# Performance work log

Measured on AMD Instinct MI355X. Metric: run time of the kernel, lower is better.

Reference implementation:

```python
import jax, jax.numpy as jnp
import numpy as np

jax.config.update("jax_enable_x64", True)

B, N, M_EQ, D_INEQ = 64, 128, 32, 64
RHO = 1.0
THRES = 1e-5
MAX_ITERS = 5000  # safety cap (original loops until relative objective change <= 1e-5)


def setup_inputs() -> dict:
    key = jax.random.key(0)
    kL, kq, kG, kA, kx0, ks = jax.random.split(key, 6)
    L = jax.random.normal(kL, (B, N, N))
    Q = jnp.einsum('bij,bkj->bik', L, L) / N + jnp.eye(N)  # SPD, well-conditioned
    q = jax.random.normal(kq, (B, N))
    G = jax.random.normal(kG, (B, D_INEQ, N))
    A = jax.random.normal(kA, (B, M_EQ, N))
    x0 = jax.random.normal(kx0, (B, N))
    slack = jax.random.uniform(ks, (B, D_INEQ)) + 0.1
    h = jnp.einsum('bdn,bn->bd', G, x0) + slack  # strictly feasible ineq
    b = jnp.einsum('bmn,bn->bm', A, x0)          # feasible eq
    f32 = jnp.float32
    return {"Q": Q.astype(f32), "q": q.astype(f32), "G": G.astype(f32),
            "h": h.astype(f32), "A": A.astype(f32), "b": b.astype(f32)}


def _alt_diff_batch(Q, q, G, h, A, b):
    """Batched Alt-Diff ADMM QP solve; returns (x [B,n], dx/dq [B,n,n])."""
    Bb, n = q.shape
    d = h.shape[1]
    m = b.shape[1]
    dt = Q.dtype
    AtA = jnp.einsum('bmi,bmj->bij', A, A)
    GtG = jnp.einsum('bdi,bdj->bij', G, G)
    R = -jnp.linalg.inv(Q + RHO * AtA + RHO * GtG)
    ATb = RHO * jnp.einsum('bmn,bm->bn', A, b)
    GTh = RHO * jnp.einsum('bdn,bd->bn', G, h)
    eye = jnp.eye(n, dtype=dt)

    def obj(x):
        return 0.5 * jnp.einsum('bi,bij,bj->b', x, Q, x) + jnp.einsum('bi,bi->b', q, x)

    init = dict(
        xk=jnp.zeros((Bb, n), dt), sk=jnp.zeros((Bb, d), dt),
        lamb=jnp.zeros((Bb, m), dt), nu=jnp.zeros((Bb, d), dt),
        dxk=jnp.zeros((Bb, n, n), dt), dsk=jnp.zeros((Bb, d, n), dt),
        dlamb=jnp.zeros((Bb, m, n), dt), dnu=jnp.zeros((Bb, d, n), dt),
        res_prev=jnp.full((Bb,), 1000.0, dt),   # res = [1000, -100] init
        res_cur=jnp.full((Bb,), -100.0, dt),
        done=jnp.zeros((Bb,), bool),
        it=jnp.zeros((), jnp.int32),
    )

    def cond(s):
        return jnp.logical_and(jnp.any(~s["done"]), s["it"] < MAX_ITERS)

    def body(s):
        xk = jnp.einsum('bij,bj->bi', R,
                        q + jnp.einsum('bmn,bm->bn', A, s["lamb"])
                          + jnp.einsum('bdn,bd->bn', G, s["nu"]) - ATb
                          + RHO * jnp.einsum('bdn,bd->bn', G, s["sk"]) - GTh)
        dxk = jnp.einsum('bij,bjk->bik', R,
                         eye + jnp.einsum('bmn,bmk->bnk', A, s["dlamb"])
                             + jnp.einsum('bdn,bdk->bnk', G, s["dnu"])
                             + RHO * jnp.einsum('bdn,bdk->bnk', G, s["dsk"]))
        Gx = jnp.einsum('bdn,bn->bd', G, xk)
        sk = jax.nn.relu(-(1.0 / RHO) * s["nu"] - (Gx - h))
        sgn = (sk > 0).astype(dt)  # sgn applied to already-relu'd sk, as in source
        dsk = (-1.0 / RHO) * sgn[:, :, None] * (s["dnu"] + RHO * jnp.einsum('bdn,bnk->bdk', G, dxk))
        lamb = s["lamb"] + RHO * (jnp.einsum('bmn,bn->bm', A, xk) - b)
        dlamb = s["dlamb"] + RHO * jnp.einsum('bmn,bnk->bmk', A, dxk)
        nu = s["nu"] + RHO * (Gx + sk - h)
        dnu = s["dnu"] + RHO * (jnp.einsum('bdn,bnk->bdk', G, dxk) + dsk)
        res_new = obj(xk)

        keep = s["done"]

        def sel(old, new):
            mask = keep.reshape((-1,) + (1,) * (new.ndim - 1))
            return jnp.where(mask, old, new)

        res_prev = jnp.where(keep, s["res_prev"], s["res_cur"])
        res_cur = jnp.where(keep, s["res_cur"], res_new)
        done = keep | (jnp.abs((res_cur - res_prev) / res_prev) <= THRES)
        return dict(
            xk=sel(s["xk"], xk), sk=sel(s["sk"], sk),
            lamb=sel(s["lamb"], lamb), nu=sel(s["nu"], nu),
            dxk=sel(s["dxk"], dxk), dsk=sel(s["dsk"], dsk),
            dlamb=sel(s["dlamb"], dlamb), dnu=sel(s["dnu"], dnu),
            res_prev=res_prev, res_cur=res_cur, done=done, it=s["it"] + 1,
        )

    final = jax.lax.while_loop(cond, body, init)
    return final["xk"], final["dxk"]


def reference(Q, q, G, h, A, b):
    out_dtype = q.dtype
    f64 = jnp.float64
    x, _dx = _alt_diff_batch(Q.astype(f64), q.astype(f64), G.astype(f64),
                             h.astype(f64), A.astype(f64), b.astype(f64))
    return x.astype(out_dtype)
```

## Files before the change

### kernel.cpp

```cpp
#include <hip/hip_runtime.h>

#define NN 128
#define ME 32
#define DI 64
#define NZ 96
#define ROWD 130
#define MAXIT 5000

#define OFF_UN 16640
#define ROWB  (OFF_UN)
#define COLB  (OFF_UN + 256)
#define PPK   (OFF_UN)
#define ZEXL  (OFF_UN + 512)
#define ZEXH  (OFF_UN + 640)
#define TVX   (OFF_UN + 704)
#define TV16  (OFF_UN + 832)
#define FLG   (OFF_UN + 864)
#define YBUF  (OFF_UN)
#define KBUF  (OFF_UN + 1536)
#define CPART (OFF_UN + 1024)
#define VP    (OFF_UN + 1280)
#define BASEV (OFF_UN + 1792)
#define QBV   (OFF_UN + 1888)
#define FPART (OFF_UN + 1024)
#define RHSV  (OFF_UN + 1280)
#define XPART (OFF_UN + 1408)
#define CB    (OFF_UN + 2688)
#define QBUF  (OFF_UN + 2816)
#define V1    (OFF_UN + 2944)
#define V2    (OFF_UN + 3072)
#define HB    (OFF_UN + 3200)
#define BB    (OFF_UN + 3264)
#define CST   (OFF_UN + 3296)
#define ZBF   (OFF_UN + 3304)
#define LDS_DBL (OFF_UN + 3400)

typedef __attribute__((ext_vector_type(2))) float f32x2;

__device__ __forceinline__ float rlf(float v, int lane) {
  return __uint_as_float((unsigned)__builtin_amdgcn_readlane((int)__float_as_uint(v), lane));
}
__device__ __forceinline__ f32x2 fma2(f32x2 a, f32x2 b, f32x2 c) {
  return __builtin_elementwise_fma(a, b, c);
}

#define MV2(PA, ZS, L0) {                                                  \
    f32x2 z0 = { rlf(ZS, L0), rlf(ZS, (L0)+1) };                           \
    A0 = fma2(Kp[PA], z0, A0); B0 = fma2(Kp2[PA], z0, B0);                 \
    f32x2 z1 = { rlf(ZS, (L0)+2), rlf(ZS, (L0)+3) };                       \
    A1 = fma2(Kp[(PA)+1], z1, A1); B1 = fma2(Kp2[(PA)+1], z1, B1); }

__global__ __launch_bounds__(320, 1) void altdiff_kernel(
    const float* __restrict__ Qg, const float* __restrict__ qg,
    const float* __restrict__ Gg, const float* __restrict__ hg,
    const float* __restrict__ Ag, const float* __restrict__ bg,
    float* __restrict__ out)
{
  extern __shared__ double ldsd[];

  const int bidx = blockIdx.x;
  const int tid  = threadIdx.x;
  const int w    = tid >> 6;
  const int l    = tid & 63;
  const int lm   = l & 31;
  const int ia   = tid & 127;
  const int hh   = tid >> 7;

  const float* Qb = Qg + (size_t)bidx * NN * NN;
  const float* Ab = Ag + (size_t)bidx * ME * NN;
  const float* Gb = Gg + (size_t)bidx * DI * NN;
  const float* qb = qg + (size_t)bidx * NN;
  const float* hb = hg + (size_t)bidx * DI;
  const float* bv = bg + (size_t)bidx * ME;

  if (tid < DI) ldsd[HB + tid] = (double)hb[tid];
  else if (tid < DI + ME) ldsd[BB + tid - DI] = (double)bv[tid - DI];
  if (tid >= 128 && tid < 256) ldsd[QBUF + tid - 128] = (double)qb[tid - 128];

  const int r = tid >> 4, c = tid & 15;
  double acc[8][8];

  if (tid < 256) {
    const float4* Q4 = (const float4*)Qb;
#pragma unroll
    for (int rr = 0; rr < 8; ++rr) {
      float4 q0 = Q4[((8*r+rr) << 5) + 2*c];
      float4 q1 = Q4[((8*r+rr) << 5) + 2*c + 1];
      acc[rr][0]=(double)q0.x; acc[rr][1]=(double)q0.y; acc[rr][2]=(double)q0.z; acc[rr][3]=(double)q0.w;
      acc[rr][4]=(double)q1.x; acc[rr][5]=(double)q1.y; acc[rr][6]=(double)q1.z; acc[rr][7]=(double)q1.w;
    }
    const float4* A4 = (const float4*)Ab;
    for (int m = 0; m < ME; ++m) {
      float4 u0 = A4[(m << 5) + 2*r], u1 = A4[(m << 5) + 2*r + 1];
      float4 v0 = A4[(m << 5) + 2*c], v1 = A4[(m << 5) + 2*c + 1];
      double uu[8] = {(double)u0.x,(double)u0.y,(double)u0.z,(double)u0.w,
                      (double)u1.x,(double)u1.y,(double)u1.z,(double)u1.w};
      double vv[8] = {(double)v0.x,(double)v0.y,(double)v0.z,(double)v0.w,
                      (double)v1.x,(double)v1.y,(double)v1.z,(double)v1.w};
#pragma unroll
      for (int rr = 0; rr < 8; ++rr)
#pragma unroll
        for (int cc = 0; cc < 8; ++cc)
          acc[rr][cc] = fma(uu[rr], vv[cc], acc[rr][cc]);
    }
    const float4* G4 = (const float4*)Gb;
    for (int d = 0; d < DI; ++d) {
      float4 u0 = G4[(d << 5) + 2*r], u1 = G4[(d << 5) + 2*r + 1];
      float4 v0 = G4[(d << 5) + 2*c], v1 = G4[(d << 5) + 2*c + 1];
      double uu[8] = {(double)u0.x,(double)u0.y,(double)u0.z,(double)u0.w,
                      (double)u1.x,(double)u1.y,(double)u1.z,(double)u1.w};
      double vv[8] = {(double)v0.x,(double)v0.y,(double)v0.z,(double)v0.w,
                      (double)v1.x,(double)v1.y,(double)v1.z,(double)v1.w};
#pragma unroll
      for (int rr = 0; rr < 8; ++rr)
#pragma unroll
        for (int cc = 0; cc < 8; ++cc)
          acc[rr][cc] = fma(uu[rr], vv[cc], acc[rr][cc]);
    }
  }

  if (tid < 256) {
    if (r == 0) {
#pragma unroll
      for (int cc = 0; cc < 8; ++cc) ldsd[ROWB + 8*c + cc] = acc[0][cc];
    }
    if (c == 0) {
#pragma unroll
      for (int rr = 0; rr < 8; ++rr) ldsd[COLB + 8*r + rr] = acc[rr][0];
    }
  }
  __syncthreads();
  for (int k = 0; k < NN; ++k) {
    if (tid < 256) {
      const int pb = (k & 1) << 7;
      const int krt = k >> 3, kcl = k & 7;
      double rowk[8], colv[8];
#pragma unroll
      for (int cc = 0; cc < 8; ++cc) rowk[cc] = ldsd[ROWB + pb + 8*c + cc];
#pragma unroll
      for (int rr = 0; rr < 8; ++rr) colv[rr] = ldsd[COLB + pb + 8*r + rr];
      const double dkk  = ldsd[ROWB + pb + k];
      const double rcpd = 1.0 / dkk;
      double rdv[8];
#pragma unroll
      for (int cc = 0; cc < 8; ++cc) rdv[cc] = rowk[cc] * rcpd;
      const bool pivR = (r == krt), pivC = (c == krt);
#pragma unroll
      for (int rr = 0; rr < 8; ++rr) {
        const double cv = colv[rr] * rcpd;
        const bool pr = pivR && (rr == kcl);
#pragma unroll
        for (int cc = 0; cc < 8; ++cc) {
          double gen = fma(-cv, rowk[cc], acc[rr][cc]);
          acc[rr][cc] = pr ? rdv[cc] : gen;
        }
      }
      if (pivC) {
#pragma unroll
        for (int cc = 0; cc < 8; ++cc) if (cc == kcl) {
#pragma unroll
          for (int rr = 0; rr < 8; ++rr) {
            const bool pr2 = pivR && (rr == kcl);
            acc[rr][cc] = pr2 ? -rcpd : colv[rr] * rcpd;
          }
        }
      }
      if (k < NN - 1) {
        const int pb2 = ((k + 1) & 1) << 7;
        const int krt2 = (k + 1) >> 3, kcl2 = (k + 1) & 7;
        if (r == krt2) {
#pragma unroll
          for (int rr = 0; rr < 8; ++rr) if (rr == kcl2) {
#pragma unroll
            for (int cc = 0; cc < 8; ++cc) ldsd[ROWB + pb2 + 8*c + cc] = acc[rr][cc];
          }
        }
        if (c == krt2) {
#pragma unroll
          for (int cc = 0; cc < 8; ++cc) if (cc == kcl2) {
#pragma unroll
            for (int rr = 0; rr < 8; ++rr) ldsd[COLB + pb2 + 8*r + rr] = acc[rr][cc];
          }
        }
      }
    }
    __syncthreads();
  }
  if (tid < 256) {
#pragma unroll
    for (int rr = 0; rr < 8; ++rr) {
      double2* dst = (double2*)(ldsd + (8*r+rr)*ROWD + 8*c);
#pragma unroll
      for (int t = 0; t < 4; ++t) dst[t] = make_double2(acc[rr][2*t], acc[rr][2*t+1]);
    }
  }
  __syncthreads();

  f32x2 Kp[12], Kp2[12];
  for (int blk = 0; blk < 8; ++blk) {
    if (tid < 256) {
      const float* gp[6];
#pragma unroll
      for (int jj = 0; jj < 6; ++jj) {
        int it = 12*blk + 6*hh + jj;
        gp[jj] = (it < DI) ? (Gb + it*NN) : (Ab + (it - DI)*NN);
      }
      double a2[6] = {0,0,0,0,0,0};
#pragma unroll 4
      for (int t = 0; t < NN; ++t) {
        double rv = ldsd[t*ROWD + ia];
#pragma unroll
        for (int jj = 0; jj < 6; ++jj)
          a2[jj] = fma(rv, (double)gp[jj][t], a2[jj]);
      }
      double2* yst = (double2*)(ldsd + YBUF + ia*12 + 6*hh);
#pragma unroll
      for (int p = 0; p < 3; ++p) yst[p] = make_double2(a2[2*p], a2[2*p+1]);
    }
    __syncthreads();
    if (tid < 256) {
      const int r2 = (ia < NZ) ? ia : 0;
      const float* brow = (r2 < DI) ? (Gb + r2*NN) : (Ab + (r2 - DI)*NN);
      double a2[6] = {0,0,0,0,0,0};
#pragma unroll 4
      for (int t = 0; t < NN; ++t) {
        double bvv = (double)brow[t];
        const double2* yr = (const double2*)(ldsd + YBUF + t*12 + 6*hh);
        double2 y0 = yr[0], y1 = yr[1], y2 = yr[2];
        a2[0] = fma(bvv, y0.x, a2[0]); a2[1] = fma(bvv, y0.y, a2[1]);
        a2[2] = fma(bvv, y1.x, a2[2]); a2[3] = fma(bvv, y1.y, a2[3]);
        a2[4] = fma(bvv, y2.x, a2[4]); a2[5] = fma(bvv, y2.y, a2[5]);
      }
      if (ia < NZ) {
#pragma unroll
        for (int jj = 0; jj < 6; ++jj) ldsd[KBUF + (6*hh + jj)*NZ + ia] = a2[jj];
      }
    }
    __syncthreads();
    if (w == (blk >> 1)) {
      if ((blk & 1) == 0) {
#pragma unroll
        for (int p = 0; p < 6; ++p) {
          Kp [p].x = (float)ldsd[KBUF + (2*p  )*NZ + l];
          Kp [p].y = (float)ldsd[KBUF + (2*p+1)*NZ + l];
          Kp2[p].x = (float)ldsd[KBUF + (2*p  )*NZ + 64 + lm];
          Kp2[p].y = (float)ldsd[KBUF + (2*p+1)*NZ + 64 + lm];
        }
      } else {
#pragma unroll
        for (int p = 0; p < 6; ++p) {
          Kp [6+p].x = (float)ldsd[KBUF + (2*p  )*NZ + l];
          Kp [6+p].y = (float)ldsd[KBUF + (2*p+1)*NZ + l];
          Kp2[6+p].x = (float)ldsd[KBUF + (2*p  )*NZ + 64 + lm];
          Kp2[6+p].y = (float)ldsd[KBUF + (2*p+1)*NZ + 64 + lm];
        }
      }
    }
    __syncthreads();
  }

  if (tid < 256) {
    double s = 0;
#pragma unroll 8
    for (int jc = 0; jc < 48; ++jc) {
      int j = 48*hh + jc;
      double coef = (j < DI) ? ldsd[HB + j] : ldsd[BB + j - DI];
      const float* src = (j < DI) ? (Gb + j*NN) : (Ab + (j - DI)*NN);
      s = fma(-(double)src[ia], coef, s);
    }
    ldsd[CPART + hh*128 + ia] = s;
  }
  __syncthreads();
  if (tid < NN) ldsd[CB + tid] = ldsd[QBUF + tid] + ldsd[CPART + tid] + ldsd[CPART + 128 + tid];
  __syncthreads();

  if (tid < 256) {
    double a = 0, b2 = 0;
#pragma unroll 4
    for (int tt = 0; tt < 64; ++tt) {
      int t = 64*hh + tt;
      double rv = ldsd[t*ROWD + ia];
      a  = fma(rv, ldsd[CB + t], a);
      b2 = fma(rv, ldsd[QBUF + t], b2);
    }
    ldsd[VP + hh*128 + ia] = a;
    ldsd[VP + 256 + hh*128 + ia] = b2;
  }
  __syncthreads();
  if (tid < NN) {
    ldsd[V1 + tid] = ldsd[VP + tid] + ldsd[VP + 128 + tid];
    ldsd[V2 + tid] = ldsd[VP + 256 + tid] + ldsd[VP + 384 + tid];
  }
  __syncthreads();

  if (tid < 256) {
    const int r2 = (ia < NZ) ? ia : 0;
    const float* brow = (r2 < DI) ? (Gb + r2*NN) : (Ab + (r2 - DI)*NN);
    const int voff = hh ? V2 : V1;
    double s = 0;
#pragma unroll 4
    for (int t = 0; t < NN; ++t) s = fma((double)brow[t], ldsd[voff + t], s);
    if (ia < NZ) ldsd[(hh ? QBV : BASEV) + ia] = s;
  }
  if (w == 0) {
    double pc = ldsd[V1+l]*ldsd[CB+l]   + ldsd[V1+64+l]*ldsd[CB+64+l];
    double pq = ldsd[V1+l]*ldsd[QBUF+l] + ldsd[V1+64+l]*ldsd[QBUF+64+l];
#pragma unroll
    for (int off = 32; off >= 1; off >>= 1) { pc += __shfl_xor(pc, off); pq += __shfl_xor(pq, off); }
    if (l == 0) { ldsd[CST] = pc; ldsd[CST+1] = pq; }
  }
  __syncthreads();

  const double baseA = ldsd[BASEV + l];
  const double baseB = ldsd[BASEV + 64 + lm];
  const double qvA   = ldsd[QBV + l];
  const double qvB   = ldsd[QBV + 64 + lm];
  const double hb2   = ldsd[HB + l] - baseA;
  const double bb2   = baseB - ldsd[BB + lm];
  const double S_uc  = ldsd[CST], S_qu = ldsd[CST + 1];
  double hnb = hb2, lb = bb2;
  double zlo = 0.0, zhi = 0.0;
  double zAlo = 0.0, zAhi = 0.0, zBlo = 0.0, zBhi = 0.0, zClo = 0.0, zChi = 0.0;
  double res_prev = 1000.0, res_cur = -100.0;

  {
    if (w < 4) ((float2*)&ldsd[PPK + (w << 6) + l])[0] = make_float2(0.f, 0.f);
    if (w == 0) ldsd[ZEXL + 64 + l] = 0.0;
    if (w == 3 && l < 32) ldsd[ZEXH + 32 + l] = 0.0;
    if (tid == 0) { ldsd[FLG] = 0.0; ldsd[FLG + 1] = 0.0; }
  }

  for (int it = 0; it < MAXIT + 3; ++it) {
    __syncthreads();
    const int buf = it & 1, nbuf = buf ^ 1;
    const int bprev = nbuf;
    const double fl = ldsd[FLG + bprev];

    if (w < 4) {
      const float2* pb = (const float2*)(ldsd + PPK + buf*256);
      float2 v0 = pb[l], v1 = pb[64 + l], v2 = pb[128 + l], v3 = pb[192 + l];
      double t = 0.0, lamn = 0.0;
      float zflo = 0.f, zfhi = 0.f;
      if (w != 3) {
        float s = (v0.x + v1.x) + (v2.x + v3.x);
        t = hnb - (double)s;
        zflo = (float)fabs(t);
      }
      if (w >= 2) {
        float sh = (v0.y + v1.y) + (v2.y + v3.y);
        lamn = lb + (double)sh;
        zfhi = (float)lamn;
      }
      if (it >= 3 && fl != 0.0) break;
      if (w == 0) { zClo = zBlo; zBlo = zAlo; zAlo = zlo; }
      if (w == 3) { zChi = zBhi; zBhi = zAhi; zAhi = zhi; }
      if (it < MAXIT) {
        if (w == 0) { zlo = fabs(t); ldsd[ZEXL + buf*64 + l] = zlo; }
        if (w != 3) hnb = hb2 + fmin(t, 0.0);
        if (w == 3) { zhi = lamn; if (l < 32) ldsd[ZEXH + buf*32 + l] = lamn; }
        if (w >= 2) lb = lamn + bb2;
        f32x2 A0 = {0.f, 0.f}, A1 = A0, B0 = A0, B1 = A0;
        if (w == 0) {
          MV2(0, zflo, 0)  MV2(2, zflo, 4)  MV2(4, zflo, 8)
          MV2(6, zflo, 12) MV2(8, zflo, 16) MV2(10, zflo, 20)
        } else if (w == 1) {
          MV2(0, zflo, 24) MV2(2, zflo, 28) MV2(4, zflo, 32)
          MV2(6, zflo, 36) MV2(8, zflo, 40) MV2(10, zflo, 44)
        } else if (w == 2) {
          MV2(0, zflo, 48) MV2(2, zflo, 52) MV2(4, zflo, 56) MV2(6, zflo, 60)
          MV2(8, zfhi, 0)  MV2(10, zfhi, 4)
        } else {
          MV2(0, zfhi, 8)  MV2(2, zfhi, 12) MV2(4, zfhi, 16)
          MV2(6, zfhi, 20) MV2(8, zfhi, 24) MV2(10, zfhi, 28)
        }
        f32x2 As = A0 + A1, Bs = B0 + B1;
        ((float2*)&ldsd[PPK + nbuf*256 + (w << 6) + l])[0] =
            make_float2(As.x + As.y, Bs.x + Bs.y);
      }
    } else {
      const float2* pb = (const float2*)(ldsd + PPK + buf*256);
      float2 v0 = pb[l], v1 = pb[64 + l], v2 = pb[128 + l], v3 = pb[192 + l];
      const double zAl = ldsd[ZEXL + bprev*64 + l];
      const double zAh = ldsd[ZEXH + bprev*32 + lm];
      const int g = l & 15;
      const double* tq = ldsd + TVX + bprev*64;
      double a0 = tq[g], a1 = tq[g + 16], a2 = tq[g + 32], a3 = tq[g + 48];
      double t1v[16];
      const double2* tp = (const double2*)(ldsd + TV16 + bprev*16);
#pragma unroll
      for (int u = 0; u < 8; ++u) { double2 vv = tp[u]; t1v[2*u] = vv.x; t1v[2*u+1] = vv.y; }
      if (it >= 3 && fl != 0.0) break;
      if (it < MAXIT) {
        float slo_f = (v0.x + v1.x) + (v2.x + v3.x);
        float shi_f = (v0.y + v1.y) + (v2.y + v3.y);
        double yf  = (double)slo_f + baseA;
        double tvl = fma(qvA, zAl, -0.5*(zAl*(baseA + yf) + yf*yf));
        double yfB = (double)shi_f + baseB;
        double tvh = fma(qvB, zAh, -0.5*(zAh*(baseB + yfB) + yfB*yfB));
        ldsd[TVX + buf*64 + l] = tvl + ((l < 32) ? tvh : 0.0);
      }
      if (l < 16 && it >= 1 && it <= MAXIT)
        ldsd[TV16 + buf*16 + l] = (a0 + a1) + (a2 + a3);
      if (it >= 2 && it <= MAXIT + 1) {
        double s1 = ((t1v[0] + t1v[1]) + (t1v[2] + t1v[3])) + ((t1v[4] + t1v[5]) + (t1v[6] + t1v[7]));
        double s2 = ((t1v[8] + t1v[9]) + (t1v[10] + t1v[11])) + ((t1v[12] + t1v[13]) + (t1v[14] + t1v[15]));
        double obj = (s1 + s2) - 0.5*S_uc + S_qu;
        res_prev = res_cur; res_cur = obj;
        if (l == 0)
          ldsd[FLG + buf] = (fabs(res_cur - res_prev) <= 1e-5 * fabs(res_prev)) ? 1.0 : 0.0;
      }
    }
  }

  if (w == 0) ldsd[ZBF + l] = zClo;
  if (w == 3 && l < 32) ldsd[ZBF + 64 + l] = zChi;
  __syncthreads();
  if (tid < 256) {
    double s = 0;
#pragma unroll 8
    for (int jc = 0; jc < 48; ++jc) {
      int j = 48*hh + jc;
      double zj = ldsd[ZBF + j];
      const float* src = (j < DI) ? (Gb + j*NN) : (Ab + (j - DI)*NN);
      s = fma((double)src[ia], zj, s);
    }
    ldsd[FPART + hh*128 + ia] = s;
  }
  __syncthreads();
  if (tid < NN) ldsd[RHSV + tid] = ldsd[CB + tid] + ldsd[FPART + tid] + ldsd[FPART + 128 + tid];
  __syncthreads();
  if (tid < 256) {
    double s = 0;
#pragma unroll 4
    for (int tt = 0; tt < 64; ++tt) {
      int t = 64*hh + tt;
      s = fma(ldsd[t*ROWD + ia], ldsd[RHSV + t], s);
    }
    ldsd[XPART + hh*128 + ia] = s;
  }
  __syncthreads();
  if (tid < NN)
    out[(size_t)bidx * NN + tid] = (float)(ldsd[XPART + tid] + ldsd[XPART + 128 + tid]);
}

extern "C" void kernel_launch(void* const* d_in, const int* in_sizes, int n_in,
                              void* d_out, int out_size, void* d_ws, size_t ws_size,
                              hipStream_t stream) {
  (void)in_sizes; (void)n_in; (void)out_size; (void)d_ws; (void)ws_size;
  const float* Q = (const float*)d_in[0];
  const float* q = (const float*)d_in[1];
  const float* G = (const float*)d_in[2];
  const float* h = (const float*)d_in[3];
  const float* A = (const float*)d_in[4];
  const float* b = (const float*)d_in[5];
  float* out = (float*)d_out;
  const size_t lds_bytes = (size_t)LDS_DBL * sizeof(double);
  altdiff_kernel<<<dim3(64), dim3(320), lds_bytes, stream>>>(Q, q, G, h, A, b, out);
}
```

Baseline: 706.9 us.

## Split ADMM matvec over two waves instead of four, shrink block to 256

The iterative ADMM loop's 96x96 matvec is now spread across 2 waves holding 24 register pairs each instead of 4 waves with 12. Each wave keeps its own partial in registers and reads only the other wave's partial from LDS. The objective work moves from one wave to waves 2 and 3, and the block shrinks from 320 to 256 threads, so the old guards on the top 64 threads go away. The aim is to cut cross-wave partial-sum traffic and per-iteration sync cost. The trade-off is twice the serial FMA chain per wave and more register pressure.

New measurement: 631.0 us. -10.7%, faster.

```diff
diff --git a/kernel.cpp b/kernel.cpp
--- a/kernel.cpp
+++ b/kernel.cpp
@@ -11,11 +11,11 @@
 #define ROWB  (OFF_UN)
 #define COLB  (OFF_UN + 256)
 #define PPK   (OFF_UN)
-#define ZEXL  (OFF_UN + 512)
-#define ZEXH  (OFF_UN + 640)
-#define TVX   (OFF_UN + 704)
-#define TV16  (OFF_UN + 832)
-#define FLG   (OFF_UN + 864)
+#define ZEXL  (OFF_UN + 256)
+#define ZEXH  (OFF_UN + 384)
+#define TVX   (OFF_UN + 448)
+#define TV16  (OFF_UN + 576)
+#define FLG   (OFF_UN + 608)
 #define YBUF  (OFF_UN)
 #define KBUF  (OFF_UN + 1536)
 #define CPART (OFF_UN + 1024)
@@ -50,7 +50,15 @@
     f32x2 z1 = { rlf(ZS, (L0)+2), rlf(ZS, (L0)+3) };                       \
     A1 = fma2(Kp[(PA)+1], z1, A1); B1 = fma2(Kp2[(PA)+1], z1, B1); }
 
-__global__ __launch_bounds__(320, 1) void altdiff_kernel(
+#define CPY12(LB)                                                          \
+  _Pragma("unroll") for (int p = 0; p < 6; ++p) {                          \
+    Kp [(LB)+p].x = (float)ldsd[KBUF + (2*p  )*NZ + l];                    \
+    Kp [(LB)+p].y = (float)ldsd[KBUF + (2*p+1)*NZ + l];                    \
+    Kp2[(LB)+p].x = (float)ldsd[KBUF + (2*p  )*NZ + 64 + lm];              \
+    Kp2[(LB)+p].y = (float)ldsd[KBUF + (2*p+1)*NZ + 64 + lm];              \
+  }
+
+__global__ __launch_bounds__(256, 1) void altdiff_kernel(
     const float* __restrict__ Qg, const float* __restrict__ qg,
     const float* __restrict__ Gg, const float* __restrict__ hg,
     const float* __restrict__ Ag, const float* __restrict__ bg,
@@ -75,12 +83,12 @@
 
   if (tid < DI) ldsd[HB + tid] = (double)hb[tid];
   else if (tid < DI + ME) ldsd[BB + tid - DI] = (double)bv[tid - DI];
-  if (tid >= 128 && tid < 256) ldsd[QBUF + tid - 128] = (double)qb[tid - 128];
+  if (tid >= 128) ldsd[QBUF + tid - 128] = (double)qb[tid - 128];
 
   const int r = tid >> 4, c = tid & 15;
   double acc[8][8];
 
-  if (tid < 256) {
+  {
     const float4* Q4 = (const float4*)Qb;
 #pragma unroll
     for (int rr = 0; rr < 8; ++rr) {
@@ -119,7 +127,7 @@
     }
   }
 
-  if (tid < 256) {
+  {
     if (r == 0) {
 #pragma unroll
       for (int cc = 0; cc < 8; ++cc) ldsd[ROWB + 8*c + cc] = acc[0][cc];
@@ -128,10 +136,8 @@
 #pragma unroll
       for (int rr = 0; rr < 8; ++rr) ldsd[COLB + 8*r + rr] = acc[rr][0];
     }
-  }
-  __syncthreads();
-  for (int k = 0; k < NN; ++k) {
-    if (tid < 256) {
+    __syncthreads();
+    for (int k = 0; k < NN; ++k) {
       const int pb = (k & 1) << 7;
       const int krt = k >> 3, kcl = k & 7;
       double rowk[8], colv[8];
@@ -183,10 +189,8 @@
           }
         }
       }
-    }
-    __syncthreads();
-  }
-  if (tid < 256) {
+      __syncthreads();
+    }
 #pragma unroll
     for (int rr = 0; rr < 8; ++rr) {
       double2* dst = (double2*)(ldsd + (8*r+rr)*ROWD + 8*c);
@@ -196,9 +200,9 @@
   }
   __syncthreads();
 
-  f32x2 Kp[12], Kp2[12];
+  f32x2 Kp[24], Kp2[24];
   for (int blk = 0; blk < 8; ++blk) {
-    if (tid < 256) {
+    {
       const float* gp[6];
 #pragma unroll
       for (int jj = 0; jj < 6; ++jj) {
@@ -218,7 +222,7 @@
       for (int p = 0; p < 3; ++p) yst[p] = make_double2(a2[2*p], a2[2*p+1]);
     }
     __syncthreads();
-    if (tid < 256) {
+    {
       const int r2 = (ia < NZ) ? ia : 0;
       const float* brow = (r2 < DI) ? (Gb + r2*NN) : (Ab + (r2 - DI)*NN);
       double a2[6] = {0,0,0,0,0,0};
@@ -237,29 +241,21 @@
       }
     }
     __syncthreads();
-    if (w == (blk >> 1)) {
-      if ((blk & 1) == 0) {
-#pragma unroll
-        for (int p = 0; p < 6; ++p) {
-          Kp [p].x = (float)ldsd[KBUF + (2*p  )*NZ + l];
-          Kp [p].y = (float)ldsd[KBUF + (2*p+1)*NZ + l];
-          Kp2[p].x = (float)ldsd[KBUF + (2*p  )*NZ + 64 + lm];
-          Kp2[p].y = (float)ldsd[KBUF + (2*p+1)*NZ + 64 + lm];
-        }
-      } else {
-#pragma unroll
-        for (int p = 0; p < 6; ++p) {
-          Kp [6+p].x = (float)ldsd[KBUF + (2*p  )*NZ + l];
-          Kp [6+p].y = (float)ldsd[KBUF + (2*p+1)*NZ + l];
-          Kp2[6+p].x = (float)ldsd[KBUF + (2*p  )*NZ + 64 + lm];
-          Kp2[6+p].y = (float)ldsd[KBUF + (2*p+1)*NZ + 64 + lm];
-        }
-      }
+    if (w == 0) {
+      if (blk == 0)      { CPY12(0) }
+      else if (blk == 1) { CPY12(6) }
+      else if (blk == 2) { CPY12(12) }
+      else if (blk == 3) { CPY12(18) }
+    } else if (w == 1) {
+      if (blk == 4)      { CPY12(0) }
+      else if (blk == 5) { CPY12(6) }
+      else if (blk == 6) { CPY12(12) }
+      else if (blk == 7) { CPY12(18) }
     }
     __syncthreads();
   }
 
-  if (tid < 256) {
+  {
     double s = 0;
 #pragma unroll 8
     for (int jc = 0; jc < 48; ++jc) {
@@ -274,7 +270,7 @@
   if (tid < NN) ldsd[CB + tid] = ldsd[QBUF + tid] + ldsd[CPART + tid] + ldsd[CPART + 128 + tid];
   __syncthreads();
 
-  if (tid < 256) {
+  {
     double a = 0, b2 = 0;
 #pragma unroll 4
     for (int tt = 0; tt < 64; ++tt) {
@@ -293,7 +289,7 @@
   }
   __syncthreads();
 
-  if (tid < 256) {
+  {
     const int r2 = (ia < NZ) ? ia : 0;
     const float* brow = (r2 < DI) ? (Gb + r2*NN) : (Ab + (r2 - DI)*NN);
     const int voff = hh ? V2 : V1;
@@ -322,11 +318,12 @@
   double zlo = 0.0, zhi = 0.0;
   double zAlo = 0.0, zAhi = 0.0, zBlo = 0.0, zBhi = 0.0, zClo = 0.0, zChi = 0.0;
   double res_prev = 1000.0, res_cur = -100.0;
-
-  {
-    if (w < 4) ((float2*)&ldsd[PPK + (w << 6) + l])[0] = make_float2(0.f, 0.f);
+  float2 own = make_float2(0.f, 0.f);
+
+  {
+    if (w < 2) *(float2*)&ldsd[PPK + w*64 + l] = make_float2(0.f, 0.f);
     if (w == 0) ldsd[ZEXL + 64 + l] = 0.0;
-    if (w == 3 && l < 32) ldsd[ZEXH + 32 + l] = 0.0;
+    if (w == 1 && l < 32) ldsd[ZEXH + 32 + l] = 0.0;
     if (tid == 0) { ldsd[FLG] = 0.0; ldsd[FLG + 1] = 0.0; }
   }
 
@@ -336,63 +333,55 @@
     const int bprev = nbuf;
     const double fl = ldsd[FLG + bprev];
 
-    if (w < 4) {
-      const float2* pb = (const float2*)(ldsd + PPK + buf*256);
-      float2 v0 = pb[l], v1 = pb[64 + l], v2 = pb[128 + l], v3 = pb[192 + l];
-      double t = 0.0, lamn = 0.0;
-      float zflo = 0.f, zfhi = 0.f;
-      if (w != 3) {
-        float s = (v0.x + v1.x) + (v2.x + v3.x);
-        t = hnb - (double)s;
-        zflo = (float)fabs(t);
-      }
-      if (w >= 2) {
-        float sh = (v0.y + v1.y) + (v2.y + v3.y);
-        lamn = lb + (double)sh;
+    if (w < 2) {
+      float2 rem = *(const float2*)&ldsd[PPK + buf*128 + (w ^ 1)*64 + l];
+      float slo = own.x + rem.x;
+      double t = hnb - (double)slo;
+      float zflo = (float)fabs(t);
+      float zfhi = 0.f;
+      double lamn = 0.0;
+      if (w == 1) {
+        float shi = own.y + rem.y;
+        lamn = lb + (double)shi;
         zfhi = (float)lamn;
       }
       if (it >= 3 && fl != 0.0) break;
       if (w == 0) { zClo = zBlo; zBlo = zAlo; zAlo = zlo; }
-      if (w == 3) { zChi = zBhi; zBhi = zAhi; zAhi = zhi; }
+      else        { zChi = zBhi; zBhi = zAhi; zAhi = zhi; }
       if (it < MAXIT) {
         if (w == 0) { zlo = fabs(t); ldsd[ZEXL + buf*64 + l] = zlo; }
-        if (w != 3) hnb = hb2 + fmin(t, 0.0);
-        if (w == 3) { zhi = lamn; if (l < 32) ldsd[ZEXH + buf*32 + l] = lamn; }
-        if (w >= 2) lb = lamn + bb2;
+        hnb = hb2 + fmin(t, 0.0);
+        if (w == 1) {
+          zhi = lamn; lb = lamn + bb2;
+          if (l < 32) ldsd[ZEXH + buf*32 + l] = lamn;
+        }
         f32x2 A0 = {0.f, 0.f}, A1 = A0, B0 = A0, B1 = A0;
         if (w == 0) {
-          MV2(0, zflo, 0)  MV2(2, zflo, 4)  MV2(4, zflo, 8)
-          MV2(6, zflo, 12) MV2(8, zflo, 16) MV2(10, zflo, 20)
-        } else if (w == 1) {
-          MV2(0, zflo, 24) MV2(2, zflo, 28) MV2(4, zflo, 32)
-          MV2(6, zflo, 36) MV2(8, zflo, 40) MV2(10, zflo, 44)
-        } else if (w == 2) {
-          MV2(0, zflo, 48) MV2(2, zflo, 52) MV2(4, zflo, 56) MV2(6, zflo, 60)
-          MV2(8, zfhi, 0)  MV2(10, zfhi, 4)
+          MV2(0,  zflo, 0)  MV2(2,  zflo, 4)  MV2(4,  zflo, 8)  MV2(6,  zflo, 12)
+          MV2(8,  zflo, 16) MV2(10, zflo, 20) MV2(12, zflo, 24) MV2(14, zflo, 28)
+          MV2(16, zflo, 32) MV2(18, zflo, 36) MV2(20, zflo, 40) MV2(22, zflo, 44)
         } else {
-          MV2(0, zfhi, 8)  MV2(2, zfhi, 12) MV2(4, zfhi, 16)
-          MV2(6, zfhi, 20) MV2(8, zfhi, 24) MV2(10, zfhi, 28)
+          MV2(0,  zflo, 48) MV2(2,  zflo, 52) MV2(4,  zflo, 56) MV2(6,  zflo, 60)
+          MV2(8,  zfhi, 0)  MV2(10, zfhi, 4)  MV2(12, zfhi, 8)  MV2(14, zfhi, 12)
+          MV2(16, zfhi, 16) MV2(18, zfhi, 20) MV2(20, zfhi, 24) MV2(22, zfhi, 28)
         }
         f32x2 As = A0 + A1, Bs = B0 + B1;
-        ((float2*)&ldsd[PPK + nbuf*256 + (w << 6) + l])[0] =
-            make_float2(As.x + As.y, Bs.x + Bs.y);
-      }
-    } else {
-      const float2* pb = (const float2*)(ldsd + PPK + buf*256);
-      float2 v0 = pb[l], v1 = pb[64 + l], v2 = pb[128 + l], v3 = pb[192 + l];
+        float2 np = make_float2(As.x + As.y, Bs.x + Bs.y);
+        *(float2*)&ldsd[PPK + nbuf*128 + w*64 + l] = np;
+        own = np;
+      }
+    } else if (w == 2) {
+      const float2* pb = (const float2*)(ldsd + PPK + buf*128);
+      float2 v0 = pb[l], v1 = pb[64 + l];
       const double zAl = ldsd[ZEXL + bprev*64 + l];
       const double zAh = ldsd[ZEXH + bprev*32 + lm];
       const int g = l & 15;
       const double* tq = ldsd + TVX + bprev*64;
       double a0 = tq[g], a1 = tq[g + 16], a2 = tq[g + 32], a3 = tq[g + 48];
-      double t1v[16];
-      const double2* tp = (const double2*)(ldsd + TV16 + bprev*16);
-#pragma unroll
-      for (int u = 0; u < 8; ++u) { double2 vv = tp[u]; t1v[2*u] = vv.x; t1v[2*u+1] = vv.y; }
       if (it >= 3 && fl != 0.0) break;
       if (it < MAXIT) {
-        float slo_f = (v0.x + v1.x) + (v2.x + v3.x);
-        float shi_f = (v0.y + v1.y) + (v2.y + v3.y);
+        float slo_f = v0.x + v1.x;
+        float shi_f = v0.y + v1.y;
         double yf  = (double)slo_f + baseA;
         double tvl = fma(qvA, zAl, -0.5*(zAl*(baseA + yf) + yf*yf));
         double yfB = (double)shi_f + baseB;
@@ -401,6 +390,12 @@
       }
       if (l < 16 && it >= 1 && it <= MAXIT)
         ldsd[TV16 + buf*16 + l] = (a0 + a1) + (a2 + a3);
+    } else {
+      double t1v[16];
+      const double2* tp = (const double2*)(ldsd + TV16 + bprev*16);
+#pragma unroll
+      for (int u = 0; u < 8; ++u) { double2 vv = tp[u]; t1v[2*u] = vv.x; t1v[2*u+1] = vv.y; }
+      if (it >= 3 && fl != 0.0) break;
       if (it >= 2 && it <= MAXIT + 1) {
         double s1 = ((t1v[0] + t1v[1]) + (t1v[2] + t1v[3])) + ((t1v[4] + t1v[5]) + (t1v[6] + t1v[7]));
         double s2 = ((t1v[8] + t1v[9]) + (t1v[10] + t1v[11])) + ((t1v[12] + t1v[13]) + (t1v[14] + t1v[15]));
@@ -413,9 +408,9 @@
   }
 
   if (w == 0) ldsd[ZBF + l] = zClo;
-  if (w == 3 && l < 32) ldsd[ZBF + 64 + l] = zChi;
-  __syncthreads();
-  if (tid < 256) {
+  if (w == 1 && l < 32) ldsd[ZBF + 64 + l] = zChi;
+  __syncthreads();
+  {
     double s = 0;
 #pragma unroll 8
     for (int jc = 0; jc < 48; ++jc) {
@@ -429,7 +424,7 @@
   __syncthreads();
   if (tid < NN) ldsd[RHSV + tid] = ldsd[CB + tid] + ldsd[FPART + tid] + ldsd[FPART + 128 + tid];
   __syncthreads();
-  if (tid < 256) {
+  {
     double s = 0;
 #pragma unroll 4
     for (int tt = 0; tt < 64; ++tt) {
@@ -455,5 +450,5 @@
   const float* b = (const float*)d_in[5];
   float* out = (float*)d_out;
   const size_t lds_bytes = (size_t)LDS_DBL * sizeof(double);
-  altdiff_kernel<<<dim3(64), dim3(320), lds_bytes, stream>>>(Q, q, G, h, A, b, out);
+  altdiff_kernel<<<dim3(64), dim3(256), lds_bytes, stream>>>(Q, q, G, h, A, b, out);
 }
```
